# Kernel tuning notes

Measured on AMD Instinct MI355X. Metric: run time of the kernel, lower is better.

Reference implementation:

```python
import jax, jax.numpy as jnp
import numpy as np

B, C, S, HID = 64, 512, 28, 256  # batch, channels, spatial size, LSTM hidden


def _param(k, shape):
    return jax.random.normal(k, shape, jnp.float32) * 0.05


def setup_inputs() -> dict:
    key = jax.random.key(0)
    ks = jax.random.split(key, 19)
    inp = {"x": jax.random.normal(ks[0], (B, C, S, S), jnp.float32)}
    # vertical bidirectional LSTM (input C, hidden HID), torch gate order i,f,g,o
    inp["v_wih_f"] = _param(ks[1], (4 * HID, C))
    inp["v_whh_f"] = _param(ks[2], (4 * HID, HID))
    inp["v_b_f"] = _param(ks[3], (4 * HID,))
    inp["v_wih_b"] = _param(ks[4], (4 * HID, C))
    inp["v_whh_b"] = _param(ks[5], (4 * HID, HID))
    inp["v_b_b"] = _param(ks[6], (4 * HID,))
    # horizontal bidirectional LSTM (input 2*HID=512, hidden HID)
    inp["h_wih_f"] = _param(ks[7], (4 * HID, 2 * HID))
    inp["h_whh_f"] = _param(ks[8], (4 * HID, HID))
    inp["h_b_f"] = _param(ks[9], (4 * HID,))
    inp["h_wih_b"] = _param(ks[10], (4 * HID, 2 * HID))
    inp["h_whh_b"] = _param(ks[11], (4 * HID, HID))
    inp["h_b_b"] = _param(ks[12], (4 * HID,))
    # 1x1 conv 512 -> 100 (10x10 attention kernel logits)
    inp["conv_w"] = _param(ks[13], (100, 2 * HID))
    inp["conv_b"] = _param(ks[14], (100,))
    return inp


def _lstm_scan(xs, wih, whh, b):
    # xs: [T, N, D] -> h sequence [T, N, HID]
    hdim = whh.shape[1]
    def step(carry, xt):
        h, c = carry
        gates = xt @ wih.T + h @ whh.T + b  # [N, 4H]
        i, f, g, o = jnp.split(gates, 4, axis=-1)
        c = jax.nn.sigmoid(f) * c + jax.nn.sigmoid(i) * jnp.tanh(g)
        h = jax.nn.sigmoid(o) * jnp.tanh(c)
        return (h, c), h
    n = xs.shape[1]
    z = jnp.zeros((n, hdim), xs.dtype)
    _, hs = jax.lax.scan(step, (z, z), xs)
    return hs


def _bilstm(x, wf, uf, bf, wb, ub, bb):
    # x: [N, T, D] -> [N, T, 2*HID]
    xs = jnp.swapaxes(x, 0, 1)
    hf = _lstm_scan(xs, wf, uf, bf)
    hb = _lstm_scan(xs[::-1], wb, ub, bb)[::-1]
    return jnp.swapaxes(jnp.concatenate([hf, hb], axis=-1), 0, 1)


def reference(x, v_wih_f, v_whh_f, v_b_f, v_wih_b, v_whh_b, v_b_b,
              h_wih_f, h_whh_f, h_b_f, h_wih_b, h_whh_b, h_b_b,
              conv_w, conv_b):
    b, c, s, _ = x.shape
    xt = jnp.transpose(x, (0, 3, 2, 1))            # [B, W, H, C]
    # vertical LSTM: seq over W, batched over (B, H)
    v_in = jnp.transpose(xt, (0, 2, 1, 3)).reshape(b * s, s, c)
    v_out = _bilstm(v_in, v_wih_f, v_whh_f, v_b_f, v_wih_b, v_whh_b, v_b_b)
    v_out = jnp.transpose(v_out.reshape(b, s, s, 2 * HID), (0, 2, 1, 3))  # [B, W, H, 512]
    # horizontal LSTM: seq over H, batched over (B, W)
    h_in = v_out.reshape(b * s, s, 2 * HID)
    h_out = _bilstm(h_in, h_wih_f, h_whh_f, h_b_f, h_wih_b, h_whh_b, h_b_b)
    feat = jnp.transpose(h_out.reshape(b, s, s, 2 * HID), (0, 3, 2, 1))  # [B, 512, H, W]
    # 1x1 conv -> [B, 100, H, W], softmax over 100 kernel entries
    kern = jnp.einsum('bfhw,of->bohw', feat, conv_w) + conv_b[None, :, None, None]
    kern = jax.nn.softmax(kern, axis=1)
    # faithful to torch: C-order reshape [B,100,H,W] -> (B*H*W, 100) kernels
    w = kern.reshape(b, s * s, 100)
    # grouped dilated conv3d == weighted sum over dilation-3 sampled 10x10 grid
    x_s = x[:, :, ::3, ::3].reshape(b, c, 100)     # [B, C, 100]
    out = jnp.einsum('bpk,bck->bpc', w, x_s)       # [B, H*W, C]
    return out.reshape(b, c, s, s)                 # faithful C-order reshape
```

## Files before the change

### kernel.cpp

```cpp
#include <hip/hip_runtime.h>
#include <hip/hip_bf16.h>
#include <stdint.h>

typedef __hip_bfloat16 bf16_t;
typedef __attribute__((ext_vector_type(8))) short short8;
typedef __attribute__((ext_vector_type(4))) float f32x4;
typedef __attribute__((ext_vector_type(4))) unsigned int u32x4;
typedef unsigned long long ull;

#define MFMA16(a, b, c) __builtin_amdgcn_mfma_f32_16x16x32_bf16(a, b, c, 0, 0, 0)

#define NROW 50176
#define NBATCH 1792

__device__ __forceinline__ void g2l16(const void* g, void* l) {
  __builtin_amdgcn_global_load_lds(
      (const __attribute__((address_space(1))) unsigned int*)g,
      (__attribute__((address_space(3))) unsigned int*)l, 16, 0, 0);
}
__device__ __forceinline__ float sigm(float x) { return 1.0f / (1.0f + __expf(-x)); }
__device__ __forceinline__ float tanh_(float x) { return 2.0f / (1.0f + __expf(-2.0f * x)) - 1.0f; }
__device__ __forceinline__ void stc(bf16_t* p, float v) { *p = __float2bfloat16(v); }
__device__ __forceinline__ void stc(float* p, float v) { *p = v; }
__device__ __forceinline__ float bf2f(unsigned short u) {
  return __uint_as_float((unsigned int)u << 16);
}

struct CvtArgs {
  const float* src[8];
  bf16_t* dst[8];
  int n[8];
};
__global__ void cvt_all(CvtArgs a) {
  int arr = blockIdx.y;
  int i = blockIdx.x * 256 + threadIdx.x;
  if (i < a.n[arr]) a.dst[arr][i] = __float2bfloat16(a.src[arr][i]);
}

__global__ void transpose_x(const float* __restrict__ x, bf16_t* __restrict__ Xin,
                            bf16_t* __restrict__ xs) {
  int c0 = blockIdx.x * 128, h = blockIdx.y, b = blockIdx.z;
  __shared__ __align__(16) short tile[128 * 29];
  const float* xb = x + ((size_t)b * 512 + c0) * 784 + h * 28;
  for (int e = threadIdx.x; e < 128 * 28; e += 256) {
    int cc = e / 28, w = e - cc * 28;
    tile[cc * 29 + w] = __bfloat16_as_short(__float2bfloat16(xb[(size_t)cc * 784 + w]));
  }
  __syncthreads();
  size_t orow0 = (size_t)(b * 28 + h) * 28;
  short* os = (short*)Xin;
  for (int e = threadIdx.x; e < 28 * 128; e += 256) {
    int w = e >> 7, cc = e & 127;
    int c = c0 + cc;
    os[(size_t)(c >> 5) * NROW * 32 + (orow0 + w) * 32 + (c & 31)] = tile[cc * 29 + w];
  }
  short* xss = (short*)xs;
  if (h % 3 == 0) {
    int kh = h / 3;
    for (int e = threadIdx.x; e < 1280; e += 256) {
      int cc = e / 10, kw = e - cc * 10;
      xss[((size_t)(b * 512) + c0 + cc) * 128 + kh * 10 + kw] = tile[cc * 29 + 3 * kw];
    }
  }
  if (h == 0) {
    for (int e = threadIdx.x; e < 128 * 28; e += 256) {
      int cc = e / 28, kp = e - cc * 28;
      xss[((size_t)(b * 512) + c0 + cc) * 128 + 100 + kp] = 0;
    }
  }
}

__global__ void pad_conv(const float* __restrict__ cw, const float* __restrict__ cb,
                         bf16_t* __restrict__ cwp, float* __restrict__ cbp,
                         unsigned int* __restrict__ bar) {
  int r = blockIdx.x;
  if (r == 0)
    for (int i = threadIdx.x; i < 7168; i += 128) bar[i] = 0;
  for (int i = threadIdx.x; i < 512; i += 128)
    cwp[r * 512 + i] = __float2bfloat16((r < 100) ? cw[r * 512 + i] : 0.0f);
  if (r == 0) cbp[threadIdx.x] = (threadIdx.x < 100) ? cb[threadIdx.x] : 0.0f;
}

template <typename CT, bool CPERM>
__global__ __launch_bounds__(256) void gemm_bt(
    const bf16_t* __restrict__ A, const bf16_t* __restrict__ B0,
    const bf16_t* __restrict__ B1, const float* __restrict__ bias0,
    const float* __restrict__ bias1, CT* __restrict__ C, int M, int N, int K) {
  __shared__ __align__(16) short smem[16384];
  short(*As)[4096] = (short(*)[4096])smem;
  short(*Bs)[4096] = (short(*)[4096])(smem + 8192);
  int tid = threadIdx.x;
  int nb = blockIdx.x;
  int bm0 = blockIdx.y * 128, bn0 = nb * 128;
  int lrow = tid >> 2, lseg = tid & 3;
  const char* Ag = (const char*)A + ((size_t)(bm0 + lrow) * 32 + lseg * 8) * 2;
  size_t Aadv = (size_t)M * 64;
  const float* biasp;
  const char *Bg1, *Bg2;
  int js = 0;
  if (CPERM) {
    int dir = nb >> 3;
    js = nb & 7;
    const bf16_t* Bsel = dir ? B1 : B0;
    biasp = dir ? bias1 : bias0;
    int br1 = (lrow >> 5) * 256 + js * 32 + (lrow & 31);
    int br2 = ((lrow + 64) >> 5) * 256 + js * 32 + (lrow & 31);
    Bg1 = (const char*)(Bsel + (size_t)br1 * K) + lseg * 16;
    Bg2 = (const char*)(Bsel + (size_t)br2 * K) + lseg * 16;
  } else {
    biasp = bias0 + bn0;
    Bg1 = (const char*)(B0 + (size_t)(bn0 + lrow) * K) + lseg * 16;
    Bg2 = Bg1 + (size_t)64 * K * 2;
  }
  int w = tid >> 6, l = tid & 63, lm = l & 15, lq = l >> 4;
  int wm = w & 1, wn = w >> 1;
  f32x4 acc[4][4] = {};
  for (int k0 = 0; k0 < K; k0 += 64) {
#pragma unroll
    for (int p = 0; p < 2; p++) {
      g2l16(Ag, (char*)As[p] + tid * 16);
      g2l16(Ag + 4096, (char*)As[p] + 4096 + tid * 16);
      g2l16(Bg1, (char*)Bs[p] + tid * 16);
      g2l16(Bg2, (char*)Bs[p] + 4096 + tid * 16);
      Ag += Aadv; Bg1 += 64; Bg2 += 64;
    }
    __syncthreads();
#pragma unroll
    for (int p = 0; p < 2; p++) {
      short8 afr[4], bfr[4];
#pragma unroll
      for (int i = 0; i < 4; i++) {
        afr[i] = *(const short8*)&As[p][(wm * 64 + i * 16 + lm) * 32 + lq * 8];
        bfr[i] = *(const short8*)&Bs[p][(wn * 64 + i * 16 + lm) * 32 + lq * 8];
      }
#pragma unroll
      for (int mi = 0; mi < 4; mi++)
#pragma unroll
        for (int ni = 0; ni < 4; ni++) acc[mi][ni] = MFMA16(afr[mi], bfr[ni], acc[mi][ni]);
    }
    __syncthreads();
  }
  float bv[4];
#pragma unroll
  for (int ni = 0; ni < 4; ni++) {
    int cb = wn * 64 + ni * 16 + lm;
    bv[ni] = CPERM ? biasp[(cb >> 5) * 256 + js * 32 + (cb & 31)] : biasp[cb];
  }
  if constexpr (sizeof(CT) == 2) {
#pragma unroll 1
    for (int mh = 0; mh < 2; mh++) {
      if (wm == mh) {
#pragma unroll
        for (int mi = 0; mi < 4; mi++)
#pragma unroll
          for (int ni = 0; ni < 4; ni++)
#pragma unroll
            for (int r = 0; r < 4; r++) {
              int row = mi * 16 + lq * 4 + r;
              int col = wn * 64 + ni * 16 + lm;
              smem[row * 130 + col] =
                  __bfloat16_as_short(__float2bfloat16(acc[mi][ni][r] + bv[ni]));
            }
      }
      __syncthreads();
      {
        int row = tid >> 2, seg = tid & 3;
        short* Crow = (short*)C + (size_t)(bm0 + mh * 64 + row) * N + bn0 + seg * 32;
#pragma unroll
        for (int j = 0; j < 4; j++)
          *(u32x4*)(Crow + j * 8) = *(const u32x4*)&smem[row * 130 + seg * 32 + j * 8];
      }
      __syncthreads();
    }
  } else {
#pragma unroll
    for (int mi = 0; mi < 4; mi++)
#pragma unroll
      for (int ni = 0; ni < 4; ni++) {
        int col = bn0 + wn * 64 + ni * 16 + lm;
#pragma unroll
        for (int r = 0; r < 4; r++) {
          size_t row = bm0 + wm * 64 + mi * 16 + lq * 4 + r;
          stc(&C[row * N + col], acc[mi][ni][r] + bv[ni]);
        }
      }
  }
}

__global__ __launch_bounds__(256, 2) void lstm_scan(
    const bf16_t* __restrict__ G, const bf16_t* __restrict__ whh_f,
    const bf16_t* __restrict__ whh_b, bf16_t* __restrict__ hA,
    bf16_t* __restrict__ hB, bf16_t* __restrict__ outb,
    unsigned int* __restrict__ bar) {
  int dir = blockIdx.y;
  int js = blockIdx.x & 7;
  int rg = blockIdx.x >> 3;
  int tid = threadIdx.x, w = tid >> 6, l = tid & 63, lm = l & 15, lq = l >> 4;
  const short* whh = (const short*)(dir ? whh_b : whh_f);
  __shared__ __align__(16) short Ws[128 * 256];
  __shared__ __align__(16) short ht[64 * 40];
#pragma unroll
  for (int i = 0; i < 16; i++) {
    int segid = i * 256 + tid;
    int row = segid >> 5, seg = segid & 31;
    int gate = row >> 5, jj = row & 31;
    short8 v = *(const short8*)&whh[((size_t)(gate * 256 + js * 32 + jj)) * 256 + seg * 8];
    *(short8*)&Ws[row * 256 + ((seg ^ (row & 7)) * 8)] = v;
  }
  __syncthreads();
  unsigned int* cnt = bar + (((dir * 28 + rg) << 2) + w) * 16;
  int r0 = rg * 64 + w * 16;
  size_t dbase = (size_t)dir * 458752;
  const unsigned short* Gb = (const unsigned short*)G + (size_t)dir * 1024 + js * 128;
  float creg[2][4] = {};
  unsigned short gvs[2][4][4];
  auto load_gvs = [&](int tt) {
#pragma unroll
    for (int nj = 0; nj < 2; nj++)
#pragma unroll
      for (int r = 0; r < 4; r++) {
        int bi = r0 + lq * 4 + r;
        const unsigned short* gp = Gb + ((size_t)bi * 28 + tt) * 2048 + nj * 16 + lm;
#pragma unroll
        for (int gate = 0; gate < 4; gate++) gvs[nj][gate][r] = gp[gate * 32];
      }
  };
  load_gvs(dir ? 27 : 0);
  int srow = w * 16 + (l >> 2), sseg = l & 3;
  int sbi = rg * 64 + srow;
  int sbb = sbi / 28, srr = sbi - sbb * 28;
#pragma unroll 1
  for (int s = 0; s < 28; s++) {
    int t = dir ? 27 - s : s;
    f32x4 acc[4][2] = {};
    if (s > 0) {
      unsigned int tgt = 8u * (unsigned)s;
      while (__hip_atomic_load(cnt, __ATOMIC_RELAXED, __HIP_MEMORY_SCOPE_AGENT) < tgt)
        __builtin_amdgcn_s_sleep(1);
      const ull* hrp = (const ull*)((s & 1) ? hA : hB);
      ull hq[8][2];
#pragma unroll
      for (int kk = 0; kk < 8; kk++) {
        size_t off = dbase + (size_t)kk * 57344 + (size_t)(r0 + lm) * 32 + lq * 8;
        hq[kk][0] =
            __hip_atomic_load(hrp + (off >> 2), __ATOMIC_RELAXED, __HIP_MEMORY_SCOPE_AGENT);
        hq[kk][1] = __hip_atomic_load(hrp + (off >> 2) + 1, __ATOMIC_RELAXED,
                                      __HIP_MEMORY_SCOPE_AGENT);
      }
#pragma unroll
      for (int kk = 0; kk < 8; kk++) {
        short8 a;
        ((ull*)&a)[0] = hq[kk][0];
        ((ull*)&a)[1] = hq[kk][1];
        int bseg = ((kk * 4 + lq) ^ (lm & 7)) * 8;
#pragma unroll
        for (int gate = 0; gate < 4; gate++)
#pragma unroll
          for (int nj = 0; nj < 2; nj++) {
            short8 b = *(const short8*)&Ws[(gate * 32 + nj * 16 + lm) * 256 + bseg];
            acc[gate][nj] = MFMA16(a, b, acc[gate][nj]);
          }
      }
    }
#pragma unroll
    for (int nj = 0; nj < 2; nj++)
#pragma unroll
      for (int r = 0; r < 4; r++) {
        float gi = bf2f(gvs[nj][0][r]) + acc[0][nj][r];
        float gf = bf2f(gvs[nj][1][r]) + acc[1][nj][r];
        float gg = bf2f(gvs[nj][2][r]) + acc[2][nj][r];
        float go = bf2f(gvs[nj][3][r]) + acc[3][nj][r];
        float cn = sigm(gf) * creg[nj][r] + sigm(gi) * tanh_(gg);
        float hn = sigm(go) * tanh_(cn);
        creg[nj][r] = cn;
        ht[(w * 16 + lq * 4 + r) * 40 + nj * 16 + lm] =
            __bfloat16_as_short(__float2bfloat16(hn));
      }
    {
      u32x4 v = *(const u32x4*)&ht[srow * 40 + sseg * 8];
      ull* hwp = (ull*)((s & 1) ? hB : hA);
      size_t off = dbase + (size_t)js * 57344 + (size_t)sbi * 32 + sseg * 8;
      ull q0 = ((const ull*)&v)[0];
      ull q1 = ((const ull*)&v)[1];
      __hip_atomic_store(hwp + (off >> 2), q0, __ATOMIC_RELAXED, __HIP_MEMORY_SCOPE_AGENT);
      __hip_atomic_store(hwp + (off >> 2) + 1, q1, __ATOMIC_RELAXED,
                         __HIP_MEMORY_SCOPE_AGENT);
      short* ob = (short*)outb + (size_t)(dir * 8 + js) * NROW * 32;
      *(u32x4*)&ob[((size_t)sbb * 784 + (size_t)t * 28 + srr) * 32 + sseg * 8] = v;
    }
    if (s < 27) {
      asm volatile("s_waitcnt vmcnt(0)" ::: "memory");
      if (l == 0)
        __hip_atomic_fetch_add(cnt, 1u, __ATOMIC_RELAXED, __HIP_MEMORY_SCOPE_AGENT);
      load_gvs(dir ? 26 - s : s + 1);
    }
  }
}

__global__ __launch_bounds__(256) void softmax_scatter(const float* __restrict__ P,
                                                       bf16_t* __restrict__ Wscr) {
  int row = blockIdx.x * 4 + (threadIdx.x >> 6);
  int l = threadIdx.x & 63;
  int b = row / 784, q = row - b * 784;
  const float* pr = P + (size_t)row * 128;
  float v0 = (l < 100) ? pr[l] : -1e30f;
  float v1 = (l + 64 < 100) ? pr[l + 64] : -1e30f;
  float m = fmaxf(v0, v1);
  for (int off = 32; off > 0; off >>= 1) m = fmaxf(m, __shfl_down(m, off));
  m = __shfl(m, 0);
  float e0 = (l < 100) ? __expf(v0 - m) : 0.0f;
  float e1 = (l + 64 < 100) ? __expf(v1 - m) : 0.0f;
  float sum = e0 + e1;
  for (int off = 32; off > 0; off >>= 1) sum += __shfl_down(sum, off);
  sum = __shfl(sum, 0);
  float inv = 1.0f / sum;
  size_t base = (size_t)b * 784 * 128;
  if (l < 100) {
    int mm = l * 784 + q;
    Wscr[base + (size_t)(mm / 100) * 128 + (mm % 100)] = __float2bfloat16(e0 * inv);
  }
  int o = l + 64;
  if (o < 100) {
    int mm = o * 784 + q;
    Wscr[base + (size_t)(mm / 100) * 128 + (mm % 100)] = __float2bfloat16(e1 * inv);
  }
}

__global__ __launch_bounds__(256) void final_gemm(const bf16_t* __restrict__ Wscr,
                                                  const bf16_t* __restrict__ xs,
                                                  float* __restrict__ outp) {
  int m0 = blockIdx.x * 112, n0 = blockIdx.y * 128, b = blockIdx.z;
  int tid = threadIdx.x, w = tid >> 6, l = tid & 63, lm = l & 15, lq = l >> 4;
  const short* Ab = (const short*)Wscr + (size_t)b * 784 * 128;
  const short* Bb = (const short*)xs + (size_t)b * 512 * 128;
  f32x4 acc[7][2] = {};
#pragma unroll
  for (int kk = 0; kk < 4; kk++) {
    short8 b0 = *(const short8*)&Bb[(size_t)(n0 + w * 32 + lm) * 128 + kk * 32 + lq * 8];
    short8 b1 = *(const short8*)&Bb[(size_t)(n0 + w * 32 + 16 + lm) * 128 + kk * 32 + lq * 8];
#pragma unroll
    for (int mi = 0; mi < 7; mi++) {
      short8 a = *(const short8*)&Ab[(size_t)(m0 + mi * 16 + lm) * 128 + kk * 32 + lq * 8];
      acc[mi][0] = MFMA16(a, b0, acc[mi][0]);
      acc[mi][1] = MFMA16(a, b1, acc[mi][1]);
    }
  }
#pragma unroll
  for (int mi = 0; mi < 7; mi++)
#pragma unroll
    for (int ni = 0; ni < 2; ni++) {
      int c = n0 + w * 32 + ni * 16 + lm;
#pragma unroll
      for (int r = 0; r < 4; r++) {
        int p = m0 + mi * 16 + lq * 4 + r;
        outp[(size_t)b * 401408 + (size_t)p * 512 + c] = acc[mi][ni][r];
      }
    }
}

extern "C" void kernel_launch(void* const* d_in, const int* in_sizes, int n_in,
                              void* d_out, int out_size, void* d_ws, size_t ws_size,
                              hipStream_t stream) {
  const float* x = (const float*)d_in[0];
  const float* v_wih_f = (const float*)d_in[1];
  const float* v_whh_f = (const float*)d_in[2];
  const float* v_b_f = (const float*)d_in[3];
  const float* v_wih_b = (const float*)d_in[4];
  const float* v_whh_b = (const float*)d_in[5];
  const float* v_b_b = (const float*)d_in[6];
  const float* h_wih_f = (const float*)d_in[7];
  const float* h_whh_f = (const float*)d_in[8];
  const float* h_b_f = (const float*)d_in[9];
  const float* h_wih_b = (const float*)d_in[10];
  const float* h_whh_b = (const float*)d_in[11];
  const float* h_b_b = (const float*)d_in[12];
  const float* conv_w = (const float*)d_in[13];
  const float* conv_b = (const float*)d_in[14];

  char* ws = (char*)d_ws;
  bf16_t* Xin = (bf16_t*)(ws);
  bf16_t* Vout = (bf16_t*)(ws + 51380224);
  bf16_t* G = (bf16_t*)(ws + 102760448);
  float* P = (float*)(ws + 102760448);
  bf16_t* Wscr = (bf16_t*)(ws + 128450560);
  bf16_t* xs = (bf16_t*)(ws + 308281344);
  bf16_t* cwp = (bf16_t*)(ws + 316669952);
  float* cbp = (float*)(ws + 316801024);
  bf16_t* hstate = (bf16_t*)(ws + 316801536);
  unsigned int* bar = (unsigned int*)(ws + 318636544);
  bf16_t* wvf = (bf16_t*)(ws + 322306560);
  bf16_t* wvb = (bf16_t*)(ws + 323355136);
  bf16_t* uvf = (bf16_t*)(ws + 324403712);
  bf16_t* uvb = (bf16_t*)(ws + 324928000);
  bf16_t* whf = (bf16_t*)(ws + 325452288);
  bf16_t* whb = (bf16_t*)(ws + 326500864);
  bf16_t* uhf = (bf16_t*)(ws + 327549440);
  bf16_t* uhb = (bf16_t*)(ws + 328073728);
  bf16_t* Hout = Xin;

  CvtArgs ca;
  ca.src[0] = v_wih_f; ca.dst[0] = wvf; ca.n[0] = 524288;
  ca.src[1] = v_wih_b; ca.dst[1] = wvb; ca.n[1] = 524288;
  ca.src[2] = v_whh_f; ca.dst[2] = uvf; ca.n[2] = 262144;
  ca.src[3] = v_whh_b; ca.dst[3] = uvb; ca.n[3] = 262144;
  ca.src[4] = h_wih_f; ca.dst[4] = whf; ca.n[4] = 524288;
  ca.src[5] = h_wih_b; ca.dst[5] = whb; ca.n[5] = 524288;
  ca.src[6] = h_whh_f; ca.dst[6] = uhf; ca.n[6] = 262144;
  ca.src[7] = h_whh_b; ca.dst[7] = uhb; ca.n[7] = 262144;
  cvt_all<<<dim3(2048, 8), 256, 0, stream>>>(ca);

  transpose_x<<<dim3(4, 28, 64), 256, 0, stream>>>(x, Xin, xs);
  pad_conv<<<dim3(128), 128, 0, stream>>>(conv_w, conv_b, cwp, cbp, bar);

  gemm_bt<bf16_t, true><<<dim3(16, 392), 256, 0, stream>>>(
      Xin, wvf, wvb, v_b_f, v_b_b, G, NROW, 2048, 512);
  lstm_scan<<<dim3(224, 2), 256, 0, stream>>>(G, uvf, uvb, hstate, Xin, Vout, bar);

  gemm_bt<bf16_t, true><<<dim3(16, 392), 256, 0, stream>>>(
      Vout, whf, whb, h_b_f, h_b_b, G, NROW, 2048, 512);
  lstm_scan<<<dim3(224, 2), 256, 0, stream>>>(G, uhf, uhb, hstate, Vout, Hout, bar + 3584);

  gemm_bt<float, false><<<dim3(1, 392), 256, 0, stream>>>(
      Hout, cwp, cwp, cbp, cbp, P, NROW, 128, 512);
  softmax_scatter<<<dim3(12544), 256, 0, stream>>>(P, Wscr);
  final_gemm<<<dim3(7, 4, 64), 256, 0, stream>>>(Wscr, xs, (float*)d_out);
}
```

Baseline: 1.007 ms.

## Fuse 1x1 conv GEMM with softmax scatter and simplify GEMM epilogue

A new conv_softmax kernel replaces the float conv GEMM plus the separate softmax_scatter kernel. It computes the 128-column logits tile, then does the row max and sum with lane shuffles and a small shared-memory exchange between the two column warps, and writes normalized bf16 weights straight into the scattered Wscr layout. This removes the fp32 P intermediate round trip and one launch. Separately, the bf16 gemm_bt epilogue no longer stages output through shared memory and stores each element directly. That risks less coalesced 2-byte stores on the two large LSTM input-projection GEMMs.

```diff
diff --git a/kernel.cpp b/kernel.cpp
--- a/kernel.cpp
+++ b/kernel.cpp
@@ -86,9 +86,8 @@
     const bf16_t* __restrict__ A, const bf16_t* __restrict__ B0,
     const bf16_t* __restrict__ B1, const float* __restrict__ bias0,
     const float* __restrict__ bias1, CT* __restrict__ C, int M, int N, int K) {
-  __shared__ __align__(16) short smem[16384];
-  short(*As)[4096] = (short(*)[4096])smem;
-  short(*Bs)[4096] = (short(*)[4096])(smem + 8192);
+  __shared__ __align__(16) short As[2][128 * 32];
+  __shared__ __align__(16) short Bs[2][128 * 32];
   int tid = threadIdx.x;
   int nb = blockIdx.x;
   int bm0 = blockIdx.y * 128, bn0 = nb * 128;
@@ -146,45 +145,144 @@
     int cb = wn * 64 + ni * 16 + lm;
     bv[ni] = CPERM ? biasp[(cb >> 5) * 256 + js * 32 + (cb & 31)] : biasp[cb];
   }
-  if constexpr (sizeof(CT) == 2) {
-#pragma unroll 1
-    for (int mh = 0; mh < 2; mh++) {
-      if (wm == mh) {
-#pragma unroll
-        for (int mi = 0; mi < 4; mi++)
-#pragma unroll
-          for (int ni = 0; ni < 4; ni++)
-#pragma unroll
-            for (int r = 0; r < 4; r++) {
-              int row = mi * 16 + lq * 4 + r;
-              int col = wn * 64 + ni * 16 + lm;
-              smem[row * 130 + col] =
-                  __bfloat16_as_short(__float2bfloat16(acc[mi][ni][r] + bv[ni]));
-            }
-      }
-      __syncthreads();
-      {
-        int row = tid >> 2, seg = tid & 3;
-        short* Crow = (short*)C + (size_t)(bm0 + mh * 64 + row) * N + bn0 + seg * 32;
-#pragma unroll
-        for (int j = 0; j < 4; j++)
-          *(u32x4*)(Crow + j * 8) = *(const u32x4*)&smem[row * 130 + seg * 32 + j * 8];
-      }
-      __syncthreads();
-    }
-  } else {
+#pragma unroll
+  for (int mi = 0; mi < 4; mi++)
+#pragma unroll
+    for (int ni = 0; ni < 4; ni++) {
+      int col = bn0 + wn * 64 + ni * 16 + lm;
+#pragma unroll
+      for (int r = 0; r < 4; r++) {
+        size_t row = bm0 + wm * 64 + mi * 16 + lq * 4 + r;
+        stc(&C[row * N + col], acc[mi][ni][r] + bv[ni]);
+      }
+    }
+}
+
+__global__ __launch_bounds__(256) void conv_softmax(
+    const bf16_t* __restrict__ A, const bf16_t* __restrict__ B0,
+    const float* __restrict__ bias, bf16_t* __restrict__ Wscr, int M, int K) {
+  __shared__ __align__(16) short As[2][128 * 32];
+  __shared__ __align__(16) short Bs[2][128 * 32];
+  __shared__ float part[2][128];
+  int tid = threadIdx.x;
+  int bm0 = blockIdx.x * 128;
+  int lrow = tid >> 2, lseg = tid & 3;
+  const char* Ag = (const char*)A + ((size_t)(bm0 + lrow) * 32 + lseg * 8) * 2;
+  size_t Aadv = (size_t)M * 64;
+  const char* Bg1 = (const char*)(B0 + (size_t)lrow * K) + lseg * 16;
+  const char* Bg2 = Bg1 + (size_t)64 * K * 2;
+  int w = tid >> 6, l = tid & 63, lm = l & 15, lq = l >> 4;
+  int wm = w & 1, wn = w >> 1;
+  f32x4 acc[4][4] = {};
+  for (int k0 = 0; k0 < K; k0 += 64) {
+#pragma unroll
+    for (int p = 0; p < 2; p++) {
+      g2l16(Ag, (char*)As[p] + tid * 16);
+      g2l16(Ag + 4096, (char*)As[p] + 4096 + tid * 16);
+      g2l16(Bg1, (char*)Bs[p] + tid * 16);
+      g2l16(Bg2, (char*)Bs[p] + 4096 + tid * 16);
+      Ag += Aadv; Bg1 += 64; Bg2 += 64;
+    }
+    __syncthreads();
+#pragma unroll
+    for (int p = 0; p < 2; p++) {
+      short8 afr[4], bfr[4];
+#pragma unroll
+      for (int i = 0; i < 4; i++) {
+        afr[i] = *(const short8*)&As[p][(wm * 64 + i * 16 + lm) * 32 + lq * 8];
+        bfr[i] = *(const short8*)&Bs[p][(wn * 64 + i * 16 + lm) * 32 + lq * 8];
+      }
+#pragma unroll
+      for (int mi = 0; mi < 4; mi++)
+#pragma unroll
+        for (int ni = 0; ni < 4; ni++) acc[mi][ni] = MFMA16(afr[mi], bfr[ni], acc[mi][ni]);
+    }
+    __syncthreads();
+  }
+  float bv[4];
+  bool vld[4];
+#pragma unroll
+  for (int ni = 0; ni < 4; ni++) {
+    int col = wn * 64 + ni * 16 + lm;
+    bv[ni] = bias[col];
+    vld[ni] = (col < 100);
+  }
+  float pmax[4][4];
+#pragma unroll
+  for (int mi = 0; mi < 4; mi++)
+#pragma unroll
+    for (int r = 0; r < 4; r++) {
+      float m = -1e30f;
+#pragma unroll
+      for (int ni = 0; ni < 4; ni++)
+        if (vld[ni]) m = fmaxf(m, acc[mi][ni][r] + bv[ni]);
+      pmax[mi][r] = m;
+    }
+#pragma unroll
+  for (int mask = 1; mask <= 8; mask <<= 1)
 #pragma unroll
     for (int mi = 0; mi < 4; mi++)
 #pragma unroll
+      for (int r = 0; r < 4; r++) pmax[mi][r] = fmaxf(pmax[mi][r], __shfl_xor(pmax[mi][r], mask));
+  if (lm == 0)
+#pragma unroll
+    for (int mi = 0; mi < 4; mi++)
+#pragma unroll
+      for (int r = 0; r < 4; r++) part[wn][wm * 64 + mi * 16 + lq * 4 + r] = pmax[mi][r];
+  __syncthreads();
+  float fm[4][4];
+#pragma unroll
+  for (int mi = 0; mi < 4; mi++)
+#pragma unroll
+    for (int r = 0; r < 4; r++)
+      fm[mi][r] = fmaxf(pmax[mi][r], part[wn ^ 1][wm * 64 + mi * 16 + lq * 4 + r]);
+  __syncthreads();
+  float ev[4][4][4];
+  float ps[4][4];
+#pragma unroll
+  for (int mi = 0; mi < 4; mi++)
+#pragma unroll
+    for (int r = 0; r < 4; r++) {
+      float s = 0.0f;
+#pragma unroll
       for (int ni = 0; ni < 4; ni++) {
-        int col = bn0 + wn * 64 + ni * 16 + lm;
-#pragma unroll
-        for (int r = 0; r < 4; r++) {
-          size_t row = bm0 + wm * 64 + mi * 16 + lq * 4 + r;
-          stc(&C[row * N + col], acc[mi][ni][r] + bv[ni]);
+        float e = vld[ni] ? __expf(acc[mi][ni][r] + bv[ni] - fm[mi][r]) : 0.0f;
+        ev[mi][ni][r] = e;
+        s += e;
+      }
+      ps[mi][r] = s;
+    }
+#pragma unroll
+  for (int mask = 1; mask <= 8; mask <<= 1)
+#pragma unroll
+    for (int mi = 0; mi < 4; mi++)
+#pragma unroll
+      for (int r = 0; r < 4; r++) ps[mi][r] += __shfl_xor(ps[mi][r], mask);
+  if (lm == 0)
+#pragma unroll
+    for (int mi = 0; mi < 4; mi++)
+#pragma unroll
+      for (int r = 0; r < 4; r++) part[wn][wm * 64 + mi * 16 + lq * 4 + r] = ps[mi][r];
+  __syncthreads();
+#pragma unroll
+  for (int mi = 0; mi < 4; mi++)
+#pragma unroll
+    for (int r = 0; r < 4; r++) {
+      float inv =
+          1.0f / (ps[mi][r] + part[wn ^ 1][wm * 64 + mi * 16 + lq * 4 + r]);
+      int grow = bm0 + wm * 64 + mi * 16 + lq * 4 + r;
+      int b = grow / 784, q = grow - b * 784;
+      size_t base = (size_t)b * 784 * 128;
+#pragma unroll
+      for (int ni = 0; ni < 4; ni++) {
+        int col = wn * 64 + ni * 16 + lm;
+        if (col < 100) {
+          int mm = col * 784 + q;
+          Wscr[base + (size_t)(mm / 100) * 128 + (mm % 100)] =
+              __float2bfloat16(ev[mi][ni][r] * inv);
         }
       }
-  }
+    }
 }
 
 __global__ __launch_bounds__(256, 2) void lstm_scan(
@@ -294,35 +392,6 @@
         __hip_atomic_fetch_add(cnt, 1u, __ATOMIC_RELAXED, __HIP_MEMORY_SCOPE_AGENT);
       load_gvs(dir ? 26 - s : s + 1);
     }
-  }
-}
-
-__global__ __launch_bounds__(256) void softmax_scatter(const float* __restrict__ P,
-                                                       bf16_t* __restrict__ Wscr) {
-  int row = blockIdx.x * 4 + (threadIdx.x >> 6);
-  int l = threadIdx.x & 63;
-  int b = row / 784, q = row - b * 784;
-  const float* pr = P + (size_t)row * 128;
-  float v0 = (l < 100) ? pr[l] : -1e30f;
-  float v1 = (l + 64 < 100) ? pr[l + 64] : -1e30f;
-  float m = fmaxf(v0, v1);
-  for (int off = 32; off > 0; off >>= 1) m = fmaxf(m, __shfl_down(m, off));
-  m = __shfl(m, 0);
-  float e0 = (l < 100) ? __expf(v0 - m) : 0.0f;
-  float e1 = (l + 64 < 100) ? __expf(v1 - m) : 0.0f;
-  float sum = e0 + e1;
-  for (int off = 32; off > 0; off >>= 1) sum += __shfl_down(sum, off);
-  sum = __shfl(sum, 0);
-  float inv = 1.0f / sum;
-  size_t base = (size_t)b * 784 * 128;
-  if (l < 100) {
-    int mm = l * 784 + q;
-    Wscr[base + (size_t)(mm / 100) * 128 + (mm % 100)] = __float2bfloat16(e0 * inv);
-  }
-  int o = l + 64;
-  if (o < 100) {
-    int mm = o * 784 + q;
-    Wscr[base + (size_t)(mm / 100) * 128 + (mm % 100)] = __float2bfloat16(e1 * inv);
   }
 }
 
@@ -381,7 +450,6 @@
   bf16_t* Xin = (bf16_t*)(ws);
   bf16_t* Vout = (bf16_t*)(ws + 51380224);
   bf16_t* G = (bf16_t*)(ws + 102760448);
-  float* P = (float*)(ws + 102760448);
   bf16_t* Wscr = (bf16_t*)(ws + 128450560);
   bf16_t* xs = (bf16_t*)(ws + 308281344);
   bf16_t* cwp = (bf16_t*)(ws + 316669952);
@@ -420,8 +488,6 @@
       Vout, whf, whb, h_b_f, h_b_b, G, NROW, 2048, 512);
   lstm_scan<<<dim3(224, 2), 256, 0, stream>>>(G, uhf, uhb, hstate, Vout, Hout, bar + 3584);
 
-  gemm_bt<float, false><<<dim3(1, 392), 256, 0, stream>>>(
-      Hout, cwp, cwp, cbp, cbp, P, NROW, 128, 512);
-  softmax_scatter<<<dim3(12544), 256, 0, stream>>>(P, Wscr);
+  conv_softmax<<<dim3(392), 256, 0, stream>>>(Hout, cwp, cbp, Wscr, NROW, 512);
   final_gemm<<<dim3(7, 4, 64), 256, 0, stream>>>(Wscr, xs, (float*)d_out);
 }
```

Result: faster. 958.4 us, median of 3 (-4.8%).
